# Performance work log

Measured on AMD Instinct MI355X. Metric: run time of the kernel, lower is better.

## Reference

```python
import jax, jax.numpy as jnp
import numpy as np

SPARSITY = 0.05
D_MODEL, HIDDEN = 1024, 64
B, S = 4, 4096

def setup_inputs() -> dict:
    key = jax.random.key(0)
    k1, k2, k3 = jax.random.split(key, 3)
    embeddings = jax.random.normal(k1, (B, S, D_MODEL), dtype=jnp.float32)
    # Kaiming-ish scaled params for the importance MLP
    W1 = jax.random.normal(k2, (D_MODEL, HIDDEN), dtype=jnp.float32) / np.sqrt(D_MODEL)
    b1 = jnp.zeros((HIDDEN,), dtype=jnp.float32)
    W2 = jax.random.normal(k3, (HIDDEN, 1), dtype=jnp.float32) / np.sqrt(HIDDEN)
    b2 = jnp.zeros((1,), dtype=jnp.float32)
    return {"embeddings": embeddings, "W1": W1, "b1": b1, "W2": W2, "b2": b2}

def reference(embeddings, W1, b1, W2, b2):
    batch_size, seq_len, _ = embeddings.shape
    k = max(1, int(seq_len * SPARSITY))
    # importance MLP -> scores [B, S]
    h = jax.nn.relu(jnp.einsum('bsd,dh->bsh', embeddings, W1) + b1)
    scores = (jnp.einsum('bsh,ho->bso', h, W2) + b2)[..., 0]
    _, top_indices = jax.lax.top_k(scores, k)  # [B, k]
    # Each row i of attention_pattern[b] has 1/k at columns top_indices[b].
    # Build [B, S] column mask once, broadcast over the query dim.
    col_mask = jnp.zeros((batch_size, seq_len), dtype=embeddings.dtype)
    col_mask = col_mask.at[jnp.arange(batch_size)[:, None], top_indices].set(1.0 / k)
    attention_pattern = jnp.broadcast_to(col_mask[:, None, :], (batch_size, seq_len, seq_len))
    return attention_pattern, top_indices
```

## Files before the change

### kernel.cpp

```cpp
#include <hip/hip_runtime.h>

#define BB 4
#define SS 4096
#define DM 1024
#define HID 64
#define KTOP 204
static constexpr size_t PATTERN_N = (size_t)BB * SS * SS;

typedef float f4 __attribute__((ext_vector_type(4)));
typedef float f32x4 __attribute__((ext_vector_type(4)));
typedef _Float16 h8v __attribute__((ext_vector_type(8)));

#define SCORES_OFF 0
#define WHF_OFF 16384
#define WLF_OFF 49152

__global__ __launch_bounds__(256) void k0_wconv(
    const float* __restrict__ W1, _Float16* __restrict__ whf,
    _Float16* __restrict__ wlf) {
  const int gid = blockIdx.x * 256 + threadIdx.x;
  const int l = gid & 63;
  const int nt = (gid >> 6) & 3;
  const int k0 = gid >> 8;
  const int kb = k0 * 32 + (l >> 4) * 8;
  const int n = nt * 16 + (l & 15);
  h8v hi, lo;
#pragma unroll
  for (int j = 0; j < 8; ++j) {
    float w = W1[(size_t)(kb + j) * HID + n] * 1024.f;
    _Float16 h = (_Float16)w;
    hi[j] = h;
    lo[j] = (_Float16)((w - (float)h) * 4096.f);
  }
  reinterpret_cast<h8v*>(whf)[(k0 * 4 + nt) * 64 + l] = hi;
  reinterpret_cast<h8v*>(wlf)[(k0 * 4 + nt) * 64 + l] = lo;
}

__global__ __launch_bounds__(256) void k1_mfma(
    const float* __restrict__ emb, const _Float16* __restrict__ whf,
    const _Float16* __restrict__ wlf, const float* __restrict__ b1,
    const float* __restrict__ W2, const float* __restrict__ b2,
    float* __restrict__ scores) {
  const int tid = threadIdx.x;
  const int l = tid & 63;
  const int wv = tid >> 6;
  const int tokw = blockIdx.x * 128 + wv * 32;
  const int lrow = l & 15;
  const int lk8 = (l >> 4) * 8;

  const float* __restrict__ ap0 = emb + (size_t)(tokw + lrow) * DM + lk8;
  const float* __restrict__ ap1 = emb + (size_t)(tokw + 16 + lrow) * DM + lk8;
  const h8v* __restrict__ bhp = reinterpret_cast<const h8v*>(whf);
  const h8v* __restrict__ blp = reinterpret_cast<const h8v*>(wlf);

  f32x4 acc0[2][4], acc1[2][4];
#pragma unroll
  for (int mt = 0; mt < 2; ++mt)
#pragma unroll
    for (int nt = 0; nt < 4; ++nt) {
      acc0[mt][nt] = (f32x4){0.f, 0.f, 0.f, 0.f};
      acc1[mt][nt] = (f32x4){0.f, 0.f, 0.f, 0.f};
    }

  f4 a0c, a1c, a0c2, a1c2;
  h8v bhc[4], blc[4];
  a0c = *reinterpret_cast<const f4*>(ap0);
  a0c2 = *reinterpret_cast<const f4*>(ap0 + 4);
  a1c = *reinterpret_cast<const f4*>(ap1);
  a1c2 = *reinterpret_cast<const f4*>(ap1 + 4);
#pragma unroll
  for (int nt = 0; nt < 4; ++nt) {
    bhc[nt] = bhp[nt * 64 + l];
    blc[nt] = blp[nt * 64 + l];
  }

#pragma unroll 2
  for (int k0 = 0; k0 < 32; ++k0) {
    f4 a0n, a1n, a0n2, a1n2;
    h8v bhn[4], bln[4];
    if (k0 < 31) {
      const int koff = (k0 + 1) * 32;
      a0n = *reinterpret_cast<const f4*>(ap0 + koff);
      a0n2 = *reinterpret_cast<const f4*>(ap0 + koff + 4);
      a1n = *reinterpret_cast<const f4*>(ap1 + koff);
      a1n2 = *reinterpret_cast<const f4*>(ap1 + koff + 4);
#pragma unroll
      for (int nt = 0; nt < 4; ++nt) {
        bhn[nt] = bhp[((k0 + 1) * 4 + nt) * 64 + l];
        bln[nt] = blp[((k0 + 1) * 4 + nt) * 64 + l];
      }
    }
    h8v ah[2], al[2];
#pragma unroll
    for (int j = 0; j < 4; ++j) {
      _Float16 h;
      h = (_Float16)a0c[j];  ah[0][j] = h;
      al[0][j] = (_Float16)((a0c[j] - (float)h) * 4096.f);
      h = (_Float16)a0c2[j]; ah[0][4 + j] = h;
      al[0][4 + j] = (_Float16)((a0c2[j] - (float)h) * 4096.f);
      h = (_Float16)a1c[j];  ah[1][j] = h;
      al[1][j] = (_Float16)((a1c[j] - (float)h) * 4096.f);
      h = (_Float16)a1c2[j]; ah[1][4 + j] = h;
      al[1][4 + j] = (_Float16)((a1c2[j] - (float)h) * 4096.f);
    }
#pragma unroll
    for (int mt = 0; mt < 2; ++mt)
#pragma unroll
      for (int nt = 0; nt < 4; ++nt) {
        acc0[mt][nt] = __builtin_amdgcn_mfma_f32_16x16x32_f16(
            ah[mt], bhc[nt], acc0[mt][nt], 0, 0, 0);
        acc1[mt][nt] = __builtin_amdgcn_mfma_f32_16x16x32_f16(
            al[mt], bhc[nt], acc1[mt][nt], 0, 0, 0);
        acc1[mt][nt] = __builtin_amdgcn_mfma_f32_16x16x32_f16(
            ah[mt], blc[nt], acc1[mt][nt], 0, 0, 0);
      }
    if (k0 < 31) {
      a0c = a0n; a0c2 = a0n2; a1c = a1n; a1c2 = a1n2;
#pragma unroll
      for (int nt = 0; nt < 4; ++nt) { bhc[nt] = bhn[nt]; blc[nt] = bln[nt]; }
    }
  }

  float w2v[4], b1v[4];
#pragma unroll
  for (int nt = 0; nt < 4; ++nt) {
    w2v[nt] = W2[nt * 16 + lrow];
    b1v[nt] = b1[nt * 16 + lrow];
  }
  const float bb2 = b2[0];
#pragma unroll
  for (int mt = 0; mt < 2; ++mt)
#pragma unroll
    for (int i = 0; i < 4; ++i) {
      float p = 0.f;
#pragma unroll
      for (int nt = 0; nt < 4; ++nt) {
        float hs = (acc0[mt][nt][i] + 0x1p-12f * acc1[mt][nt][i]) * 0x1p-10f +
                   b1v[nt];
        hs = hs > 0.f ? hs : 0.f;
        p = fmaf(hs, w2v[nt], p);
      }
      p += __shfl_xor(p, 1, 64);
      p += __shfl_xor(p, 2, 64);
      p += __shfl_xor(p, 4, 64);
      p += __shfl_xor(p, 8, 64);
      if (lrow == 0)
        scores[tokw + mt * 16 + (l >> 4) * 4 + i] = p + bb2;
    }
}

__global__ __launch_bounds__(256) void k2_topk(
    const float* __restrict__ scores, float* __restrict__ out_idx) {
  __shared__ __align__(16) float sc[SS];
  __shared__ int red[256];
  const int tid = threadIdx.x;
  const int b = blockIdx.x >> 6;
  const int ic = blockIdx.x & 63;
  const float* row = scores + (size_t)b * SS;
#pragma unroll
  for (int q = 0; q < 4; ++q) {
    int f = tid + q * 256;
    *reinterpret_cast<f4*>(&sc[f * 4]) =
        *reinterpret_cast<const f4*>(&row[f * 4]);
  }
  __syncthreads();
  const int il = tid & 63;
  const int part = tid >> 6;
  const int i = ic * 64 + il;
  const float si = sc[i];
  const f4* s4 = reinterpret_cast<const f4*>(sc);
  int cnt = 0;
  for (int j4 = part * 256; j4 < part * 256 + 256; ++j4) {
    f4 v = s4[j4];
    int j = j4 * 4;
    cnt += (int)(v.x > si) + (int)((v.x == si) & (j + 0 < i));
    cnt += (int)(v.y > si) + (int)((v.y == si) & (j + 1 < i));
    cnt += (int)(v.z > si) + (int)((v.z == si) & (j + 2 < i));
    cnt += (int)(v.w > si) + (int)((v.w == si) & (j + 3 < i));
  }
  red[tid] = cnt;
  __syncthreads();
  if (tid < 64) {
    int tot = red[tid] + red[tid + 64] + red[tid + 128] + red[tid + 192];
    if (tot < KTOP) out_idx[b * KTOP + tot] = (float)(ic * 64 + tid);
  }
}

__global__ __launch_bounds__(256) void k3_pattern(
    const float* __restrict__ out_idx, float* __restrict__ pat) {
  __shared__ __align__(16) float mask[SS];
  const int tid = threadIdx.x;
  const int b  = blockIdx.x >> 8;
  const int r0 = (blockIdx.x & 255) * 16;
  const f4 zero = (f4){0.f, 0.f, 0.f, 0.f};
#pragma unroll
  for (int q = 0; q < 4; ++q) {
    int f = tid + q * 256;
    *reinterpret_cast<f4*>(&mask[f * 4]) = zero;
  }
  __syncthreads();
  if (tid < KTOP) {
    int c = (int)out_idx[b * KTOP + tid];
    mask[c] = 1.0f / (float)KTOP;
  }
  __syncthreads();
  const f4 m0 = *reinterpret_cast<const f4*>(&mask[(tid)*4]);
  const f4 m1 = *reinterpret_cast<const f4*>(&mask[(tid + 256) * 4]);
  const f4 m2 = *reinterpret_cast<const f4*>(&mask[(tid + 512) * 4]);
  const f4 m3 = *reinterpret_cast<const f4*>(&mask[(tid + 768) * 4]);
  for (int r = 0; r < 16; ++r) {
    f4* p4 = reinterpret_cast<f4*>(pat + ((size_t)b * SS + r0 + r) * SS);
    __builtin_nontemporal_store(m0, &p4[tid]);
    __builtin_nontemporal_store(m1, &p4[tid + 256]);
    __builtin_nontemporal_store(m2, &p4[tid + 512]);
    __builtin_nontemporal_store(m3, &p4[tid + 768]);
  }
}

extern "C" void kernel_launch(void* const* d_in, const int* in_sizes, int n_in,
                              void* d_out, int out_size, void* d_ws,
                              size_t ws_size, hipStream_t stream) {
  const float* emb = (const float*)d_in[0];
  const float* W1  = (const float*)d_in[1];
  const float* b1  = (const float*)d_in[2];
  const float* W2  = (const float*)d_in[3];
  const float* b2  = (const float*)d_in[4];
  float* out = (float*)d_out;
  float* pat     = out;
  float* out_idx = out + PATTERN_N;
  float* scores = out + SCORES_OFF;
  _Float16* whf = (_Float16*)(out + WHF_OFF);
  _Float16* wlf = (_Float16*)(out + WLF_OFF);

  k0_wconv<<<dim3(32), dim3(256), 0, stream>>>(W1, whf, wlf);
  k1_mfma<<<dim3((BB * SS) / 128), dim3(256), 0, stream>>>(emb, whf, wlf, b1,
                                                           W2, b2, scores);
  k2_topk<<<dim3(BB * (SS / 64)), dim3(256), 0, stream>>>(scores, out_idx);
  k3_pattern<<<dim3((BB * SS) / 16), dim3(256), 0, stream>>>(out_idx, pat);
}
```

Baseline: 121.5 us.

## Split MLP hidden dim across waves and quadruple k1 grid size

The score kernel now gives each block 32 tokens instead of 128. Each of the 4 waves computes one 16-column slice of the 64-wide hidden layer, and the partial scores are reduced across waves through shared memory. The main loop is rewritten with explicit double-buffered loads, and occupancy is hinted via launch bounds. This raises the block count from 128 to 512 to fill more CUs and cuts per-wave register pressure, at the cost of all 4 waves rereading the same embedding rows (4x redundant A loads and conversions) plus an added barrier. Total runtime is likely dominated by the 268MB pattern write, so the effect on end-to-end time is small.

Result: slower. 133.6 us (+9.9%).

```diff
diff --git a/kernel.cpp b/kernel.cpp
--- a/kernel.cpp
+++ b/kernel.cpp
@@ -36,117 +36,107 @@
   reinterpret_cast<h8v*>(wlf)[(k0 * 4 + nt) * 64 + l] = lo;
 }
 
-__global__ __launch_bounds__(256) void k1_mfma(
+#define LOAD_SET(KK, A, BH, BL)                         \
+  {                                                     \
+    const int koff_ = (KK) * 32;                        \
+    A##0 = *reinterpret_cast<const f4*>(ap0 + koff_);   \
+    A##1 = *reinterpret_cast<const f4*>(ap0 + koff_ + 4); \
+    A##2 = *reinterpret_cast<const f4*>(ap1 + koff_);   \
+    A##3 = *reinterpret_cast<const f4*>(ap1 + koff_ + 4); \
+    BH = bhp0[(size_t)(KK) * 256];                      \
+    BL = blp0[(size_t)(KK) * 256];                      \
+  }
+
+#define CONV4(SRC, DSTH, DSTL, O)                       \
+  {                                                     \
+    _Float16 h_;                                        \
+    float x_;                                           \
+    x_ = SRC[0]; h_ = (_Float16)x_; DSTH[O + 0] = h_;   \
+    DSTL[O + 0] = (_Float16)((x_ - (float)h_) * 4096.f); \
+    x_ = SRC[1]; h_ = (_Float16)x_; DSTH[O + 1] = h_;   \
+    DSTL[O + 1] = (_Float16)((x_ - (float)h_) * 4096.f); \
+    x_ = SRC[2]; h_ = (_Float16)x_; DSTH[O + 2] = h_;   \
+    DSTL[O + 2] = (_Float16)((x_ - (float)h_) * 4096.f); \
+    x_ = SRC[3]; h_ = (_Float16)x_; DSTH[O + 3] = h_;   \
+    DSTL[O + 3] = (_Float16)((x_ - (float)h_) * 4096.f); \
+  }
+
+#define COMPUTE(A, BH, BL)                                            \
+  {                                                                   \
+    h8v ah0_, al0_, ah1_, al1_;                                       \
+    CONV4(A##0, ah0_, al0_, 0);                                       \
+    CONV4(A##1, ah0_, al0_, 4);                                       \
+    CONV4(A##2, ah1_, al1_, 0);                                       \
+    CONV4(A##3, ah1_, al1_, 4);                                       \
+    acc00 = __builtin_amdgcn_mfma_f32_16x16x32_f16(ah0_, BH, acc00, 0, 0, 0); \
+    acc10 = __builtin_amdgcn_mfma_f32_16x16x32_f16(al0_, BH, acc10, 0, 0, 0); \
+    acc10 = __builtin_amdgcn_mfma_f32_16x16x32_f16(ah0_, BL, acc10, 0, 0, 0); \
+    acc01 = __builtin_amdgcn_mfma_f32_16x16x32_f16(ah1_, BH, acc01, 0, 0, 0); \
+    acc11 = __builtin_amdgcn_mfma_f32_16x16x32_f16(al1_, BH, acc11, 0, 0, 0); \
+    acc11 = __builtin_amdgcn_mfma_f32_16x16x32_f16(ah1_, BL, acc11, 0, 0, 0); \
+  }
+
+__global__ __launch_bounds__(256, 2) void k1_mfma(
     const float* __restrict__ emb, const _Float16* __restrict__ whf,
     const _Float16* __restrict__ wlf, const float* __restrict__ b1,
     const float* __restrict__ W2, const float* __restrict__ b2,
     float* __restrict__ scores) {
+  __shared__ float lds3[4][32];
   const int tid = threadIdx.x;
   const int l = tid & 63;
   const int wv = tid >> 6;
-  const int tokw = blockIdx.x * 128 + wv * 32;
+  const int tokg = blockIdx.x * 32;
   const int lrow = l & 15;
   const int lk8 = (l >> 4) * 8;
 
-  const float* __restrict__ ap0 = emb + (size_t)(tokw + lrow) * DM + lk8;
-  const float* __restrict__ ap1 = emb + (size_t)(tokw + 16 + lrow) * DM + lk8;
-  const h8v* __restrict__ bhp = reinterpret_cast<const h8v*>(whf);
-  const h8v* __restrict__ blp = reinterpret_cast<const h8v*>(wlf);
-
-  f32x4 acc0[2][4], acc1[2][4];
-#pragma unroll
-  for (int mt = 0; mt < 2; ++mt)
-#pragma unroll
-    for (int nt = 0; nt < 4; ++nt) {
-      acc0[mt][nt] = (f32x4){0.f, 0.f, 0.f, 0.f};
-      acc1[mt][nt] = (f32x4){0.f, 0.f, 0.f, 0.f};
-    }
-
-  f4 a0c, a1c, a0c2, a1c2;
-  h8v bhc[4], blc[4];
-  a0c = *reinterpret_cast<const f4*>(ap0);
-  a0c2 = *reinterpret_cast<const f4*>(ap0 + 4);
-  a1c = *reinterpret_cast<const f4*>(ap1);
-  a1c2 = *reinterpret_cast<const f4*>(ap1 + 4);
-#pragma unroll
-  for (int nt = 0; nt < 4; ++nt) {
-    bhc[nt] = bhp[nt * 64 + l];
-    blc[nt] = blp[nt * 64 + l];
-  }
-
-#pragma unroll 2
-  for (int k0 = 0; k0 < 32; ++k0) {
-    f4 a0n, a1n, a0n2, a1n2;
-    h8v bhn[4], bln[4];
-    if (k0 < 31) {
-      const int koff = (k0 + 1) * 32;
-      a0n = *reinterpret_cast<const f4*>(ap0 + koff);
-      a0n2 = *reinterpret_cast<const f4*>(ap0 + koff + 4);
-      a1n = *reinterpret_cast<const f4*>(ap1 + koff);
-      a1n2 = *reinterpret_cast<const f4*>(ap1 + koff + 4);
-#pragma unroll
-      for (int nt = 0; nt < 4; ++nt) {
-        bhn[nt] = bhp[((k0 + 1) * 4 + nt) * 64 + l];
-        bln[nt] = blp[((k0 + 1) * 4 + nt) * 64 + l];
-      }
-    }
-    h8v ah[2], al[2];
-#pragma unroll
-    for (int j = 0; j < 4; ++j) {
-      _Float16 h;
-      h = (_Float16)a0c[j];  ah[0][j] = h;
-      al[0][j] = (_Float16)((a0c[j] - (float)h) * 4096.f);
-      h = (_Float16)a0c2[j]; ah[0][4 + j] = h;
-      al[0][4 + j] = (_Float16)((a0c2[j] - (float)h) * 4096.f);
-      h = (_Float16)a1c[j];  ah[1][j] = h;
-      al[1][j] = (_Float16)((a1c[j] - (float)h) * 4096.f);
-      h = (_Float16)a1c2[j]; ah[1][4 + j] = h;
-      al[1][4 + j] = (_Float16)((a1c2[j] - (float)h) * 4096.f);
-    }
-#pragma unroll
-    for (int mt = 0; mt < 2; ++mt)
-#pragma unroll
-      for (int nt = 0; nt < 4; ++nt) {
-        acc0[mt][nt] = __builtin_amdgcn_mfma_f32_16x16x32_f16(
-            ah[mt], bhc[nt], acc0[mt][nt], 0, 0, 0);
-        acc1[mt][nt] = __builtin_amdgcn_mfma_f32_16x16x32_f16(
-            al[mt], bhc[nt], acc1[mt][nt], 0, 0, 0);
-        acc1[mt][nt] = __builtin_amdgcn_mfma_f32_16x16x32_f16(
-            ah[mt], blc[nt], acc1[mt][nt], 0, 0, 0);
-      }
-    if (k0 < 31) {
-      a0c = a0n; a0c2 = a0n2; a1c = a1n; a1c2 = a1n2;
-#pragma unroll
-      for (int nt = 0; nt < 4; ++nt) { bhc[nt] = bhn[nt]; blc[nt] = bln[nt]; }
-    }
-  }
-
-  float w2v[4], b1v[4];
-#pragma unroll
-  for (int nt = 0; nt < 4; ++nt) {
-    w2v[nt] = W2[nt * 16 + lrow];
-    b1v[nt] = b1[nt * 16 + lrow];
-  }
-  const float bb2 = b2[0];
-#pragma unroll
-  for (int mt = 0; mt < 2; ++mt)
+  const float* __restrict__ ap0 = emb + (size_t)(tokg + lrow) * DM + lk8;
+  const float* __restrict__ ap1 = emb + (size_t)(tokg + 16 + lrow) * DM + lk8;
+  const h8v* __restrict__ bhp0 =
+      reinterpret_cast<const h8v*>(whf) + wv * 64 + l;
+  const h8v* __restrict__ blp0 =
+      reinterpret_cast<const h8v*>(wlf) + wv * 64 + l;
+
+  f32x4 acc00 = {0.f, 0.f, 0.f, 0.f}, acc01 = {0.f, 0.f, 0.f, 0.f};
+  f32x4 acc10 = {0.f, 0.f, 0.f, 0.f}, acc11 = {0.f, 0.f, 0.f, 0.f};
+
+  f4 aA0, aA1, aA2, aA3, aB0, aB1, aB2, aB3;
+  h8v bhA, blA, bhB, blB;
+
+  LOAD_SET(0, aA, bhA, blA);
+#pragma unroll 1
+  for (int kk = 0; kk < 16; ++kk) {
+    const int k0 = kk * 2;
+    const int kn2 = (k0 + 2 < 32) ? k0 + 2 : 31;
+    LOAD_SET(k0 + 1, aB, bhB, blB);
+    COMPUTE(aA, bhA, blA);
+    LOAD_SET(kn2, aA, bhA, blA);
+    COMPUTE(aB, bhB, blB);
+  }
+
+  const float b1v = b1[wv * 16 + lrow];
+  const float w2v = W2[wv * 16 + lrow];
+  f32x4 accA[2][1];
+#pragma unroll
+  for (int mt = 0; mt < 2; ++mt) {
 #pragma unroll
     for (int i = 0; i < 4; ++i) {
-      float p = 0.f;
-#pragma unroll
-      for (int nt = 0; nt < 4; ++nt) {
-        float hs = (acc0[mt][nt][i] + 0x1p-12f * acc1[mt][nt][i]) * 0x1p-10f +
-                   b1v[nt];
-        hs = hs > 0.f ? hs : 0.f;
-        p = fmaf(hs, w2v[nt], p);
-      }
+      float a0 = (mt == 0) ? acc00[i] : acc01[i];
+      float a1 = (mt == 0) ? acc10[i] : acc11[i];
+      float hs = (a0 + 0x1p-12f * a1) * 0x1p-10f + b1v;
+      hs = hs > 0.f ? hs : 0.f;
+      float p = hs * w2v;
       p += __shfl_xor(p, 1, 64);
       p += __shfl_xor(p, 2, 64);
       p += __shfl_xor(p, 4, 64);
       p += __shfl_xor(p, 8, 64);
-      if (lrow == 0)
-        scores[tokw + mt * 16 + (l >> 4) * 4 + i] = p + bb2;
+      if (lrow == 0) lds3[wv][mt * 16 + (l >> 4) * 4 + i] = p;
     }
+  }
+  __syncthreads();
+  if (tid < 32) {
+    scores[tokg + tid] = lds3[0][tid] + lds3[1][tid] + lds3[2][tid] +
+                         lds3[3][tid] + b2[0];
+  }
 }
 
 __global__ __launch_bounds__(256) void k2_topk(
@@ -233,8 +223,8 @@
   _Float16* wlf = (_Float16*)(out + WLF_OFF);
 
   k0_wconv<<<dim3(32), dim3(256), 0, stream>>>(W1, whf, wlf);
-  k1_mfma<<<dim3((BB * SS) / 128), dim3(256), 0, stream>>>(emb, whf, wlf, b1,
-                                                           W2, b2, scores);
+  k1_mfma<<<dim3((BB * SS) / 32), dim3(256), 0, stream>>>(emb, whf, wlf, b1,
+                                                          W2, b2, scores);
   k2_topk<<<dim3(BB * (SS / 64)), dim3(256), 0, stream>>>(scores, out_idx);
   k3_pattern<<<dim3((BB * SS) / 16), dim3(256), 0, stream>>>(out_idx, pat);
 }
```
